# Kernel optimization log

Measured on AMD Instinct MI355X. Metric: run time of the kernel, lower is better.

The kernel has to match this reference:

```python
import jax, jax.numpy as jnp
import numpy as np

# model dims
B_, L_ = 2, 1024
D_MODEL = 768
N_LAYER = 6
VOCAB = 32000
MAX_POS = 2048
D_INNER = 2 * D_MODEL          # expand=2 (mamba default)
D_STATE = 16
D_CONV = 4
DT_RANK = (D_MODEL + 15) // 16 # ceil(d_model/16) = 48
EPS = 1e-5
D_EMB = D_MODEL // 2


def setup_inputs() -> dict:
    key = jax.random.key(0)
    ks = jax.random.split(key, 12)
    s = 0.02
    nl = N_LAYER
    A_init = jnp.tile(jnp.log(jnp.arange(1, D_STATE + 1, dtype=jnp.float32))[None, None, :], (nl, D_INNER, 1))
    return {
        "input_ids": jax.random.randint(ks[0], (B_, L_), 0, VOCAB),
        "position_ids": jax.random.randint(ks[1], (B_, L_), 0, MAX_POS),
        "emb_w": jax.random.normal(ks[2], (VOCAB, D_EMB), jnp.float32) * s,
        "pos_emb_w": jax.random.normal(ks[3], (MAX_POS, D_MODEL - D_EMB), jnp.float32) * s,
        "norm_w": jnp.ones((nl, D_MODEL), jnp.float32),
        "in_proj_w": jax.random.normal(ks[4], (nl, 2 * D_INNER, D_MODEL), jnp.float32) * s,
        "conv_w": jax.random.normal(ks[5], (nl, D_INNER, D_CONV), jnp.float32) * s,
        "conv_b": jnp.zeros((nl, D_INNER), jnp.float32),
        "x_proj_w": jax.random.normal(ks[6], (nl, DT_RANK + 2 * D_STATE, D_INNER), jnp.float32) * s,
        "dt_proj_w": jax.random.normal(ks[7], (nl, D_INNER, DT_RANK), jnp.float32) * s,
        "dt_proj_b": jax.random.normal(ks[8], (nl, D_INNER), jnp.float32) * s,
        "A_log": A_init,
        "D_vec": jnp.ones((nl, D_INNER), jnp.float32),
        "out_proj_w": jax.random.normal(ks[9], (nl, D_MODEL, D_INNER), jnp.float32) * s,
        "norm_f_w": jnp.ones((D_MODEL,), jnp.float32),
    }


def _rmsnorm(x, w, eps=EPS):
    x = x.astype(jnp.float32)
    return x * jax.lax.rsqrt(jnp.mean(x * x, axis=-1, keepdims=True) + eps) * w


def _causal_conv1d(x, w, b):
    # x: [B, L, D], w: [D, K] depthwise, b: [D]; causal left-pad K-1
    xT = jnp.transpose(x, (0, 2, 1))  # [B, D, L]
    out = jax.lax.conv_general_dilated(
        xT, w[:, None, :], window_strides=(1,), padding=[(w.shape[-1] - 1, 0)],
        dimension_numbers=("NCH", "OIH", "NCH"), feature_group_count=w.shape[0])
    return jnp.transpose(out, (0, 2, 1)) + b


def _selective_scan(x, dt, Bm, Cm, A, Dv):
    # x, dt: [B, L, Di]; Bm, Cm: [B, L, N]; A: [Di, N]; Dv: [Di]
    def step(h, inp):
        x_t, dt_t, B_t, C_t = inp  # [B,Di], [B,Di], [B,N], [B,N]
        dA = jnp.exp(dt_t[:, :, None] * A)                       # [B,Di,N], in (0,1]
        h = dA * h + dt_t[:, :, None] * B_t[:, None, :] * x_t[:, :, None]
        y = jnp.einsum("bdn,bn->bd", h, C_t)
        return h, y

    h0 = jnp.zeros((x.shape[0], A.shape[0], A.shape[1]), x.dtype)
    xs = (jnp.swapaxes(x, 0, 1), jnp.swapaxes(dt, 0, 1),
          jnp.swapaxes(Bm, 0, 1), jnp.swapaxes(Cm, 0, 1))
    _, ys = jax.lax.scan(step, h0, xs)
    return jnp.swapaxes(ys, 0, 1) + x * Dv


def _mamba_block(hidden, residual, p):
    # Block with fused_add_norm semantics: residual += hidden; h = RMSNorm(residual); h = Mamba(h)
    norm_w, in_w, cw, cb, xp_w, dtw, dtb, A_log, Dv, ow = p
    residual = hidden + residual
    hs = _rmsnorm(residual, norm_w)
    xz = jnp.einsum("bld,ed->ble", hs, in_w)      # [B,L,2*Di]
    x, z = jnp.split(xz, 2, axis=-1)
    x = jax.nn.silu(_causal_conv1d(x, cw, cb))
    x_dbl = jnp.einsum("bld,ed->ble", x, xp_w)     # [B,L,dt_rank+2N]
    dt = x_dbl[..., :DT_RANK]
    Bm = x_dbl[..., DT_RANK:DT_RANK + D_STATE]
    Cm = x_dbl[..., DT_RANK + D_STATE:]
    dt = jax.nn.softplus(jnp.einsum("blr,dr->bld", dt, dtw) + dtb)
    A = -jnp.exp(A_log)
    y = _selective_scan(x, dt, Bm, Cm, A, Dv)
    y = y * jax.nn.silu(z)
    return jnp.einsum("bld,ed->ble", y, ow), residual


def reference(input_ids, position_ids, emb_w, pos_emb_w, norm_w, in_proj_w, conv_w,
              conv_b, x_proj_w, dt_proj_w, dt_proj_b, A_log, D_vec, out_proj_w, norm_f_w):
    # token emb (d_model//2) || position emb (d_model - d_model//2)
    hidden = jnp.concatenate([emb_w[input_ids], pos_emb_w[position_ids]], axis=-1)
    residual = jnp.zeros_like(hidden)  # residual=None on first block == 0

    def layer_step(carry, p):
        h, r = carry
        h2, r2 = _mamba_block(h, r, p)
        return (h2, r2), None

    params = (norm_w, in_proj_w, conv_w, conv_b, x_proj_w, dt_proj_w, dt_proj_b,
              A_log, D_vec, out_proj_w)
    (hidden, residual), _ = jax.lax.scan(layer_step, (hidden, residual), params)
    hs = _rmsnorm(hidden + residual, norm_f_w)
    # LM head on first d_model//2 dims, weight tied to token embedding
    logits = jnp.einsum("bld,vd->blv", hs[..., :D_EMB], emb_w)
    return logits
```

## Files before the change

kernel.cpp:

```cpp
#include <hip/hip_runtime.h>
#include <math.h>

#define B_SZ 2
#define L_SZ 1024
#define BL (B_SZ * L_SZ)
#define D_MODEL 768
#define N_LAYER 6
#define VOCAB 32000
#define D_INNER 1536
#define D_STATE 16
#define D_CONV 4
#define DT_RANK 48
#define D_EMB 384
#define EPS 1e-5f

#define NCHUNK 64
#define CT 16
#define XD (DT_RANK + 2 * D_STATE)

typedef float vfloat4 __attribute__((ext_vector_type(4)));
typedef float f32x4  __attribute__((ext_vector_type(4)));
typedef short bf16x8 __attribute__((ext_vector_type(8)));

__device__ __forceinline__ float siluf(float x) {
    return x / (1.f + __expf(-x));
}

__global__ void embed_kernel(const int* __restrict__ ids, const int* __restrict__ pos,
                             const float* __restrict__ emb, const float* __restrict__ pemb,
                             float* __restrict__ hidden, float* __restrict__ residual) {
    int idx = blockIdx.x * blockDim.x + threadIdx.x;
    if (idx >= BL * D_MODEL) return;
    int c = idx % D_MODEL;
    int t = idx / D_MODEL;
    float v;
    if (c < D_EMB) v = emb[(size_t)ids[t] * D_EMB + c];
    else           v = pemb[(size_t)pos[t] * (D_MODEL - D_EMB) + (c - D_EMB)];
    hidden[idx] = v;
    residual[idx] = 0.f;
}

__global__ __launch_bounds__(256) void add_rmsnorm_kernel(
    const float* __restrict__ hidden, float* __restrict__ residual,
    const float* __restrict__ w, float* __restrict__ out) {
    int row = blockIdx.x;
    const float* h = hidden + (size_t)row * D_MODEL;
    float* r = residual + (size_t)row * D_MODEL;
    float* o = out + (size_t)row * D_MODEL;

    float v[3];
    float ss = 0.f;
#pragma unroll
    for (int i = 0; i < 3; i++) {
        int c = threadIdx.x + i * 256;
        float x = h[c] + r[c];
        v[i] = x;
        r[c] = x;
        ss += x * x;
    }
#pragma unroll
    for (int off = 32; off > 0; off >>= 1) ss += __shfl_down(ss, off, 64);
    __shared__ float parts[4];
    __shared__ float s_scale;
    int wid = threadIdx.x >> 6;
    int lane = threadIdx.x & 63;
    if (lane == 0) parts[wid] = ss;
    __syncthreads();
    if (threadIdx.x == 0) {
        float tot = parts[0] + parts[1] + parts[2] + parts[3];
        s_scale = rsqrtf(tot / (float)D_MODEL + EPS);
    }
    __syncthreads();
    float scale = s_scale;
#pragma unroll
    for (int i = 0; i < 3; i++) {
        int c = threadIdx.x + i * 256;
        o[c] = v[i] * scale * w[c];
    }
}

__global__ __launch_bounds__(256) void frag_convert_kernel(
    const float* __restrict__ src, int R, int ld, int Ksrc, int Kt,
    short* __restrict__ dh, short* __restrict__ dl) {
    int tile = blockIdx.x;
    int kt = tile % Kt, rt = tile / Kt;
    __shared__ float fs[128][65];
    int t = threadIdx.x;
    int rr = t >> 4;
    int c4 = (t & 15) * 4;
#pragma unroll
    for (int i = 0; i < 8; i++) {
        int rloc = rr + i * 16;
        int grow = rt * 128 + rloc;
        int gk = kt * 64 + c4;
        vfloat4 v = {0.f, 0.f, 0.f, 0.f};
        if (grow < R && gk < Ksrc)
            v = *(const vfloat4*)&src[(size_t)grow * ld + gk];
        fs[rloc][c4 + 0] = v[0];
        fs[rloc][c4 + 1] = v[1];
        fs[rloc][c4 + 2] = v[2];
        fs[rloc][c4 + 3] = v[3];
    }
    __syncthreads();
#pragma unroll
    for (int i = 0; i < 4; i++) {
        int o = t + i * 256;
        int sub = o >> 6, ln = o & 63;
        int r = (sub >> 1) * 16 + (ln & 15);
        int k = (sub & 1) * 32 + (ln >> 4) * 8;
        bf16x8 h, l;
#pragma unroll
        for (int j = 0; j < 8; j++) {
            float x = fs[r][k + j];
            unsigned u = __float_as_uint(x);
            h[j] = (short)(u >> 16);
            float res = x - __uint_as_float(u & 0xffff0000u);
            l[j] = (short)(__float_as_uint(res) >> 16);
        }
        size_t doff = (size_t)tile * 8192 + (size_t)o * 8;
        *(bf16x8*)&dh[doff] = h;
        *(bf16x8*)&dl[doff] = l;
    }
}

__device__ __forceinline__ void gload16(const short* g, short* l) {
    __builtin_amdgcn_global_load_lds(
        (const __attribute__((address_space(1))) void*)g,
        (__attribute__((address_space(3))) void*)l, 16, 0, 0);
}

__global__ __launch_bounds__(256, 2) void gemm_frag_kernel(
    const short* __restrict__ Af_h, const short* __restrict__ Af_l,
    const short* __restrict__ Bf_h, const short* __restrict__ Bf_l,
    const float* __restrict__ bias, float* __restrict__ C,
    int Mt, int Nt, int Kt, int N, int act, int ksplit) {

    __shared__ __align__(16) short smem[32768];

    const int tid  = threadIdx.x;
    const int lane = tid & 63;
    const int w    = tid >> 6;
    const int wm   = w >> 1, wn = w & 1;

    int nb  = Mt * Nt;
    int bid = blockIdx.x;
    int q = nb >> 3, r = nb & 7;
    int xcd = bid & 7, lin = bid >> 3;
    int wg = (xcd < r) ? (xcd * (q + 1) + lin) : (r * (q + 1) + (xcd - r) * q + lin);
    int mt = wg % Mt;
    int nt = wg / Mt;

    const int ktn = Kt / ksplit;
    const int kt0 = blockIdx.y * ktn;

    const short* ga_h = Af_h + ((size_t)mt * Kt + kt0) * 8192;
    const short* ga_l = Af_l + ((size_t)mt * Kt + kt0) * 8192;
    const short* gb_h = Bf_h + ((size_t)nt * Kt + kt0) * 8192;
    const short* gb_l = Bf_l + ((size_t)nt * Kt + kt0) * 8192;

    f32x4 acc[4][4];
#pragma unroll
    for (int i = 0; i < 4; i++)
#pragma unroll
        for (int j = 0; j < 4; j++)
            acc[i][j] = (f32x4){0.f, 0.f, 0.f, 0.f};

    for (int kk = 0; kk < ktn; kk++) {
        __syncthreads();
        {
            const size_t tb = (size_t)kk * 8192;
#pragma unroll
            for (int i = 0; i < 4; i++) {
                const int o = w * 2048 + i * 512;
                const int go = o + lane * 8;
                gload16(ga_h + tb + go, &smem[o]);
                gload16(ga_l + tb + go, &smem[8192  + o]);
                gload16(gb_h + tb + go, &smem[16384 + o]);
                gload16(gb_l + tb + go, &smem[24576 + o]);
            }
        }
        __syncthreads();

#pragma unroll
        for (int ksub = 0; ksub < 2; ksub++) {
            bf16x8 a_h[4], a_l[4], b_h[4], b_l[4];
#pragma unroll
            for (int mi = 0; mi < 4; mi++) {
                const int off = (((wm * 4 + mi) * 2 + ksub) * 64 + lane) * 8;
                a_h[mi] = *(const bf16x8*)&smem[off];
                a_l[mi] = *(const bf16x8*)&smem[8192 + off];
            }
#pragma unroll
            for (int ni = 0; ni < 4; ni++) {
                const int off = (((wn * 4 + ni) * 2 + ksub) * 64 + lane) * 8;
                b_h[ni] = *(const bf16x8*)&smem[16384 + off];
                b_l[ni] = *(const bf16x8*)&smem[24576 + off];
            }
#pragma unroll
            for (int mi = 0; mi < 4; mi++)
#pragma unroll
                for (int ni = 0; ni < 4; ni++) {
                    acc[mi][ni] = __builtin_amdgcn_mfma_f32_16x16x32_bf16(
                        a_h[mi], b_h[ni], acc[mi][ni], 0, 0, 0);
                    acc[mi][ni] = __builtin_amdgcn_mfma_f32_16x16x32_bf16(
                        a_h[mi], b_l[ni], acc[mi][ni], 0, 0, 0);
                    acc[mi][ni] = __builtin_amdgcn_mfma_f32_16x16x32_bf16(
                        a_l[mi], b_h[ni], acc[mi][ni], 0, 0, 0);
                }
        }
    }

    const int row0 = mt * 128 + wm * 64 + ((lane >> 4) << 2);
    const int col0 = nt * 128 + wn * 64 + (lane & 15);
    if (ksplit > 1) {
#pragma unroll
        for (int ni = 0; ni < 4; ni++) {
            const int col = col0 + ni * 16;
            if (col < N) {
#pragma unroll
                for (int mi = 0; mi < 4; mi++)
#pragma unroll
                    for (int rr = 0; rr < 4; rr++)
                        atomicAdd(&C[(size_t)(row0 + mi * 16 + rr) * N + col],
                                  acc[mi][ni][rr]);
            }
        }
    } else {
#pragma unroll
        for (int ni = 0; ni < 4; ni++) {
            const int col = col0 + ni * 16;
            if (col < N) {
                const float bv = bias ? bias[col] : 0.f;
#pragma unroll
                for (int mi = 0; mi < 4; mi++) {
#pragma unroll
                    for (int rr = 0; rr < 4; rr++) {
                        const int row = row0 + mi * 16 + rr;
                        float v = acc[mi][ni][rr] + bv;
                        if (act == 1) v = (v > 20.f) ? v : log1pf(__expf(v));
                        C[(size_t)row * N + col] = v;
                    }
                }
            }
        }
    }
}

__global__ void conv_silu_kernel(const float* __restrict__ xz,
                                 const float* __restrict__ cw,
                                 const float* __restrict__ cb,
                                 float* __restrict__ out) {
    int idx = blockIdx.x * blockDim.x + threadIdx.x;
    if (idx >= BL * D_INNER) return;
    int d = idx % D_INNER;
    int t = (idx / D_INNER) % L_SZ;
    int b = idx / (D_INNER * L_SZ);
    const float* xcol = xz + (size_t)b * L_SZ * (2 * D_INNER) + d;
    float s = cb[d];
#pragma unroll
    for (int j = 0; j < D_CONV; j++) {
        int li = t - (D_CONV - 1) + j;
        if (li >= 0) s += xcol[(size_t)li * (2 * D_INNER)] * cw[d * D_CONV + j];
    }
    out[idx] = siluf(s);
}

__global__ __launch_bounds__(256) void scan_passA_kernel(
    const float* __restrict__ xconv, const float* __restrict__ dt,
    const float* __restrict__ xdbl, const float* __restrict__ A_log,
    float* __restrict__ Pbuf, float* __restrict__ Sbuf) {
    int d = blockIdx.x * 256 + threadIdx.x;
    int c = blockIdx.y;
    int b = blockIdx.z;
    int t0 = c * CT;

    __shared__ float Bsh[CT][D_STATE];
    {
        int row = threadIdx.x >> 4, n = threadIdx.x & 15;
        Bsh[row][n] = xdbl[((size_t)(b * L_SZ + t0 + row)) * XD + DT_RANK + n];
    }
    __syncthreads();

    float A[D_STATE];
#pragma unroll
    for (int n = 0; n < D_STATE; n++) A[n] = -__expf(A_log[(size_t)d * D_STATE + n]);

    float P[D_STATE], S[D_STATE];
#pragma unroll
    for (int n = 0; n < D_STATE; n++) { P[n] = 1.f; S[n] = 0.f; }

    for (int t = 0; t < CT; t++) {
        size_t row = (size_t)b * L_SZ + t0 + t;
        float dtv = dt[row * D_INNER + d];
        float xv  = xconv[row * D_INNER + d];
#pragma unroll
        for (int n = 0; n < D_STATE; n++) {
            float dA = __expf(dtv * A[n]);
            P[n] *= dA;
            S[n] = dA * S[n] + dtv * Bsh[t][n] * xv;
        }
    }
    size_t base = (((size_t)b * NCHUNK + c) * D_INNER + d) * D_STATE;
#pragma unroll
    for (int n = 0; n < D_STATE; n++) { Pbuf[base + n] = P[n]; Sbuf[base + n] = S[n]; }
}

__global__ __launch_bounds__(256) void scan_passB_kernel(
    const float* __restrict__ Pbuf, const float* __restrict__ Sbuf,
    float* __restrict__ Hbuf) {
    int idx = blockIdx.x * 256 + threadIdx.x;
    int b = idx / (D_INNER * D_STATE);
    int dn = idx % (D_INNER * D_STATE);
    const int stride = D_INNER * D_STATE;
    size_t base = (size_t)b * NCHUNK * stride + dn;
    float H = 0.f;
#pragma unroll 8
    for (int c = 0; c < NCHUNK; c++) {
        size_t off = base + (size_t)c * stride;
        float p = Pbuf[off];
        float s = Sbuf[off];
        Hbuf[off] = H;
        H = p * H + s;
    }
}

__global__ __launch_bounds__(256) void scan_passC_kernel(
    const float* __restrict__ xconv, const float* __restrict__ dt,
    const float* __restrict__ xdbl, const float* __restrict__ A_log,
    const float* __restrict__ Dv, const float* __restrict__ xz,
    const float* __restrict__ Hin,
    float* __restrict__ y) {
    int d = blockIdx.x * 256 + threadIdx.x;
    int c = blockIdx.y;
    int b = blockIdx.z;
    int t0 = c * CT;

    __shared__ float BCsh[CT][2 * D_STATE];
#pragma unroll
    for (int i = 0; i < 2; i++) {
        int idx = threadIdx.x + i * 256;
        int row = idx >> 5, col = idx & 31;
        BCsh[row][col] = xdbl[((size_t)(b * L_SZ + t0 + row)) * XD + DT_RANK + col];
    }
    __syncthreads();

    float A[D_STATE];
#pragma unroll
    for (int n = 0; n < D_STATE; n++) A[n] = -__expf(A_log[(size_t)d * D_STATE + n]);
    float Dd = Dv[d];

    float h[D_STATE];
    size_t hbase = (((size_t)b * NCHUNK + c) * D_INNER + d) * D_STATE;
#pragma unroll
    for (int n = 0; n < D_STATE; n++) h[n] = Hin[hbase + n];

    for (int t = 0; t < CT; t++) {
        size_t row = (size_t)b * L_SZ + t0 + t;
        float dtv = dt[row * D_INNER + d];
        float xv  = xconv[row * D_INNER + d];
        float acc = 0.f;
#pragma unroll
        for (int n = 0; n < D_STATE; n++) {
            float dA = __expf(dtv * A[n]);
            h[n] = dA * h[n] + dtv * BCsh[t][n] * xv;
            acc += h[n] * BCsh[t][D_STATE + n];
        }
        acc += xv * Dd;
        float zv = xz[row * (2 * D_INNER) + D_INNER + d];
        y[row * D_INNER + d] = acc * siluf(zv);
    }
}

extern "C" void kernel_launch(void* const* d_in, const int* in_sizes, int n_in,
                              void* d_out, int out_size, void* d_ws, size_t ws_size,
                              hipStream_t stream) {
    const int*   input_ids    = (const int*)d_in[0];
    const int*   position_ids = (const int*)d_in[1];
    const float* emb_w        = (const float*)d_in[2];
    const float* pos_emb_w    = (const float*)d_in[3];
    const float* norm_w       = (const float*)d_in[4];
    const float* in_proj_w    = (const float*)d_in[5];
    const float* conv_w       = (const float*)d_in[6];
    const float* conv_b       = (const float*)d_in[7];
    const float* x_proj_w     = (const float*)d_in[8];
    const float* dt_proj_w    = (const float*)d_in[9];
    const float* dt_proj_b    = (const float*)d_in[10];
    const float* A_log        = (const float*)d_in[11];
    const float* D_vec        = (const float*)d_in[12];
    const float* out_proj_w   = (const float*)d_in[13];
    const float* norm_f_w     = (const float*)d_in[14];
    float* logits = (float*)d_out;

    float* ws = (float*)d_ws;
    float* hidden   = ws; ws += (size_t)BL * D_MODEL;
    float* residual = ws; ws += (size_t)BL * D_MODEL;
    float* hs       = ws; ws += (size_t)BL * D_MODEL;
    float* xz       = ws; ws += (size_t)BL * 2 * D_INNER;
    float* xconv    = ws; ws += (size_t)BL * D_INNER;
    float* xdbl     = ws; ws += (size_t)BL * XD;
    float* dtbuf    = ws; ws += (size_t)BL * D_INNER;
    float* ybuf     = ws; ws += (size_t)BL * D_INNER;
    float* Pbuf     = ws; ws += (size_t)B_SZ * NCHUNK * D_INNER * D_STATE;
    float* Sbuf     = ws; ws += (size_t)B_SZ * NCHUNK * D_INNER * D_STATE;
    float* Hbuf     = ws; ws += (size_t)B_SZ * NCHUNK * D_INNER * D_STATE;

    short* sp = (short*)ws;
    auto salloc = [&](size_t n) { short* p = sp; sp += n; return p; };
    const int KT_DM  = D_MODEL / 64;
    const int KT_DI  = D_INNER / 64;
    const int KT_EMB = D_EMB / 64;
    short* embf_h = salloc((size_t)(VOCAB/128) * KT_EMB * 8192);
    short* embf_l = salloc((size_t)(VOCAB/128) * KT_EMB * 8192);
    short* iwf_h  = salloc((size_t)(2*D_INNER/128) * KT_DM * 8192);
    short* iwf_l  = salloc((size_t)(2*D_INNER/128) * KT_DM * 8192);
    short* xpf_h  = salloc((size_t)1 * KT_DI * 8192);
    short* xpf_l  = salloc((size_t)1 * KT_DI * 8192);
    short* dtwf_h = salloc((size_t)(D_INNER/128) * 1 * 8192);
    short* dtwf_l = salloc((size_t)(D_INNER/128) * 1 * 8192);
    short* owf_h  = salloc((size_t)(D_MODEL/128) * KT_DI * 8192);
    short* owf_l  = salloc((size_t)(D_MODEL/128) * KT_DI * 8192);
    short* hsf_h  = salloc((size_t)(BL/128) * KT_DM * 8192);
    short* hsf_l  = salloc((size_t)(BL/128) * KT_DM * 8192);
    short* xcf_h  = salloc((size_t)(BL/128) * KT_DI * 8192);
    short* xcf_l  = salloc((size_t)(BL/128) * KT_DI * 8192);
    short* x48f_h = salloc((size_t)(BL/128) * 1 * 8192);
    short* x48f_l = salloc((size_t)(BL/128) * 1 * 8192);
    short* yf_h   = salloc((size_t)(BL/128) * KT_DI * 8192);
    short* yf_l   = salloc((size_t)(BL/128) * KT_DI * 8192);

    auto conv_frag = [&](const float* src, int R, int ld, int Ksrc, int Rt, int Kt,
                         short* dh, short* dl) {
        frag_convert_kernel<<<Rt * Kt, 256, 0, stream>>>(src, R, ld, Ksrc, Kt, dh, dl);
    };
    auto gemm = [&](const short* Ah, const short* Al, const short* Bh, const short* Bl,
                    const float* bias, float* C, int Mt, int Nt, int Kt, int N,
                    int act, int ksplit) {
        dim3 grid(Mt * Nt, ksplit);
        gemm_frag_kernel<<<grid, 256, 0, stream>>>(Ah, Al, Bh, Bl, bias, C,
                                                   Mt, Nt, Kt, N, act, ksplit);
    };

    embed_kernel<<<(BL * D_MODEL + 255) / 256, 256, 0, stream>>>(
        input_ids, position_ids, emb_w, pos_emb_w, hidden, residual);

    conv_frag(emb_w, VOCAB, D_EMB, D_EMB, VOCAB / 128, KT_EMB, embf_h, embf_l);

    for (int l = 0; l < N_LAYER; l++) {
        const float* nw  = norm_w     + (size_t)l * D_MODEL;
        const float* iw  = in_proj_w  + (size_t)l * 2 * D_INNER * D_MODEL;
        const float* cw  = conv_w     + (size_t)l * D_INNER * D_CONV;
        const float* cb  = conv_b     + (size_t)l * D_INNER;
        const float* xpw = x_proj_w   + (size_t)l * XD * D_INNER;
        const float* dtw = dt_proj_w  + (size_t)l * D_INNER * DT_RANK;
        const float* dtb = dt_proj_b  + (size_t)l * D_INNER;
        const float* al  = A_log      + (size_t)l * D_INNER * D_STATE;
        const float* dv  = D_vec      + (size_t)l * D_INNER;
        const float* ow  = out_proj_w + (size_t)l * D_MODEL * D_INNER;

        add_rmsnorm_kernel<<<BL, 256, 0, stream>>>(hidden, residual, nw, hs);
        conv_frag(hs, BL, D_MODEL, D_MODEL, BL / 128, KT_DM, hsf_h, hsf_l);
        conv_frag(iw, 2 * D_INNER, D_MODEL, D_MODEL, 2 * D_INNER / 128, KT_DM,
                  iwf_h, iwf_l);

        gemm(hsf_h, hsf_l, iwf_h, iwf_l, nullptr, xz,
             BL / 128, 2 * D_INNER / 128, KT_DM, 2 * D_INNER, 0, 1);

        conv_silu_kernel<<<(BL * D_INNER + 255) / 256, 256, 0, stream>>>(xz, cw, cb, xconv);
        conv_frag(xconv, BL, D_INNER, D_INNER, BL / 128, KT_DI, xcf_h, xcf_l);
        conv_frag(xpw, XD, D_INNER, D_INNER, 1, KT_DI, xpf_h, xpf_l);

        hipMemsetAsync(xdbl, 0, (size_t)BL * XD * sizeof(float), stream);
        gemm(xcf_h, xcf_l, xpf_h, xpf_l, nullptr, xdbl,
             BL / 128, 1, KT_DI, XD, 0, 8);

        conv_frag(xdbl, BL, XD, DT_RANK, BL / 128, 1, x48f_h, x48f_l);
        conv_frag(dtw, D_INNER, DT_RANK, DT_RANK, D_INNER / 128, 1, dtwf_h, dtwf_l);
        gemm(x48f_h, x48f_l, dtwf_h, dtwf_l, dtb, dtbuf,
             BL / 128, D_INNER / 128, 1, D_INNER, 1, 1);

        {
            dim3 gA(D_INNER / 256, NCHUNK, B_SZ);
            scan_passA_kernel<<<gA, 256, 0, stream>>>(xconv, dtbuf, xdbl, al, Pbuf, Sbuf);
            scan_passB_kernel<<<(B_SZ * D_INNER * D_STATE) / 256, 256, 0, stream>>>(
                Pbuf, Sbuf, Hbuf);
            scan_passC_kernel<<<gA, 256, 0, stream>>>(xconv, dtbuf, xdbl, al, dv, xz,
                                                      Hbuf, ybuf);
        }

        conv_frag(ybuf, BL, D_INNER, D_INNER, BL / 128, KT_DI, yf_h, yf_l);
        conv_frag(ow, D_MODEL, D_INNER, D_INNER, D_MODEL / 128, KT_DI, owf_h, owf_l);
        hipMemsetAsync(hidden, 0, (size_t)BL * D_MODEL * sizeof(float), stream);
        gemm(yf_h, yf_l, owf_h, owf_l, nullptr, hidden,
             BL / 128, D_MODEL / 128, KT_DI, D_MODEL, 0, 2);
    }

    add_rmsnorm_kernel<<<BL, 256, 0, stream>>>(hidden, residual, norm_f_w, hs);
    conv_frag(hs, BL, D_MODEL, D_EMB, BL / 128, KT_EMB, hsf_h, hsf_l);

    gemm(hsf_h, hsf_l, embf_h, embf_l, nullptr, logits,
         BL / 128, VOCAB / 128, KT_EMB, VOCAB, 0, 1);
}
```

Baseline: 1.904 ms.

## Halve GEMM K-tile to raise occupancy and batch per-layer weight conversions

The GEMM K-step drops from 64 to 32, which halves the shared-memory tile and lets the launch bound allow 4 blocks per CU instead of 2. The fragment layout is re-indexed to match. The x_proj and dt_proj weight conversions are hoisted out of the layer loop into one batched launch across all layers. The xdbl memset is folded into the conv_silu kernel, and out_proj uses split-K 4. In exchange, each K step now needs twice as many barriers and global-to-LDS rounds, and split-K 4 adds more atomics.

```diff
diff --git a/kernel.cpp b/kernel.cpp
--- a/kernel.cpp
+++ b/kernel.cpp
@@ -80,10 +80,17 @@
 }
 
 __global__ __launch_bounds__(256) void frag_convert_kernel(
-    const float* __restrict__ src, int R, int ld, int Ksrc, int Kt,
+    const float* __restrict__ src, int R, int ld, int Ksrc, int Kt64,
+    size_t src_lstride, size_t dst_lstride,
     short* __restrict__ dh, short* __restrict__ dl) {
     int tile = blockIdx.x;
-    int kt = tile % Kt, rt = tile / Kt;
+    int lyr = blockIdx.y;
+    const float* s = src + (size_t)lyr * src_lstride;
+    short* dhp = dh + (size_t)lyr * dst_lstride;
+    short* dlp = dl + (size_t)lyr * dst_lstride;
+    int kt = tile % Kt64, rt = tile / Kt64;
+    const int K32 = Kt64 * 2;
+
     __shared__ float fs[128][65];
     int t = threadIdx.x;
     int rr = t >> 4;
@@ -95,7 +102,7 @@
         int gk = kt * 64 + c4;
         vfloat4 v = {0.f, 0.f, 0.f, 0.f};
         if (grow < R && gk < Ksrc)
-            v = *(const vfloat4*)&src[(size_t)grow * ld + gk];
+            v = *(const vfloat4*)&s[(size_t)grow * ld + gk];
         fs[rloc][c4 + 0] = v[0];
         fs[rloc][c4 + 1] = v[1];
         fs[rloc][c4 + 2] = v[2];
@@ -106,8 +113,9 @@
     for (int i = 0; i < 4; i++) {
         int o = t + i * 256;
         int sub = o >> 6, ln = o & 63;
-        int r = (sub >> 1) * 16 + (ln & 15);
-        int k = (sub & 1) * 32 + (ln >> 4) * 8;
+        int msub = sub >> 1, ksub = sub & 1;
+        int r = msub * 16 + (ln & 15);
+        int k = ksub * 32 + (ln >> 4) * 8;
         bf16x8 h, l;
 #pragma unroll
         for (int j = 0; j < 8; j++) {
@@ -117,9 +125,10 @@
             float res = x - __uint_as_float(u & 0xffff0000u);
             l[j] = (short)(__float_as_uint(res) >> 16);
         }
-        size_t doff = (size_t)tile * 8192 + (size_t)o * 8;
-        *(bf16x8*)&dh[doff] = h;
-        *(bf16x8*)&dl[doff] = l;
+        size_t doff = ((size_t)rt * K32 + kt * 2 + ksub) * 4096
+                    + (size_t)(msub * 64 + ln) * 8;
+        *(bf16x8*)&dhp[doff] = h;
+        *(bf16x8*)&dlp[doff] = l;
     }
 }
 
@@ -129,13 +138,13 @@
         (__attribute__((address_space(3))) void*)l, 16, 0, 0);
 }
 
-__global__ __launch_bounds__(256, 2) void gemm_frag_kernel(
+__global__ __launch_bounds__(256, 4) void gemm_frag_kernel(
     const short* __restrict__ Af_h, const short* __restrict__ Af_l,
     const short* __restrict__ Bf_h, const short* __restrict__ Bf_l,
     const float* __restrict__ bias, float* __restrict__ C,
-    int Mt, int Nt, int Kt, int N, int act, int ksplit) {
-
-    __shared__ __align__(16) short smem[32768];
+    int Mt, int Nt, int K32, int N, int act, int ksplit) {
+
+    __shared__ __align__(16) short smem[16384];
 
     const int tid  = threadIdx.x;
     const int lane = tid & 63;
@@ -150,13 +159,13 @@
     int mt = wg % Mt;
     int nt = wg / Mt;
 
-    const int ktn = Kt / ksplit;
+    const int ktn = K32 / ksplit;
     const int kt0 = blockIdx.y * ktn;
 
-    const short* ga_h = Af_h + ((size_t)mt * Kt + kt0) * 8192;
-    const short* ga_l = Af_l + ((size_t)mt * Kt + kt0) * 8192;
-    const short* gb_h = Bf_h + ((size_t)nt * Kt + kt0) * 8192;
-    const short* gb_l = Bf_l + ((size_t)nt * Kt + kt0) * 8192;
+    const short* ga_h = Af_h + ((size_t)mt * K32 + kt0) * 4096;
+    const short* ga_l = Af_l + ((size_t)mt * K32 + kt0) * 4096;
+    const short* gb_h = Bf_h + ((size_t)nt * K32 + kt0) * 4096;
+    const short* gb_l = Bf_l + ((size_t)nt * K32 + kt0) * 4096;
 
     f32x4 acc[4][4];
 #pragma unroll
@@ -168,46 +177,43 @@
     for (int kk = 0; kk < ktn; kk++) {
         __syncthreads();
         {
-            const size_t tb = (size_t)kk * 8192;
-#pragma unroll
-            for (int i = 0; i < 4; i++) {
-                const int o = w * 2048 + i * 512;
+            const size_t tb = (size_t)kk * 4096;
+#pragma unroll
+            for (int i = 0; i < 2; i++) {
+                const int o = w * 1024 + i * 512;
                 const int go = o + lane * 8;
                 gload16(ga_h + tb + go, &smem[o]);
-                gload16(ga_l + tb + go, &smem[8192  + o]);
-                gload16(gb_h + tb + go, &smem[16384 + o]);
-                gload16(gb_l + tb + go, &smem[24576 + o]);
+                gload16(ga_l + tb + go, &smem[4096  + o]);
+                gload16(gb_h + tb + go, &smem[8192  + o]);
+                gload16(gb_l + tb + go, &smem[12288 + o]);
             }
         }
         __syncthreads();
 
-#pragma unroll
-        for (int ksub = 0; ksub < 2; ksub++) {
-            bf16x8 a_h[4], a_l[4], b_h[4], b_l[4];
-#pragma unroll
-            for (int mi = 0; mi < 4; mi++) {
-                const int off = (((wm * 4 + mi) * 2 + ksub) * 64 + lane) * 8;
-                a_h[mi] = *(const bf16x8*)&smem[off];
-                a_l[mi] = *(const bf16x8*)&smem[8192 + off];
+        bf16x8 a_h[4], a_l[4], b_h[4], b_l[4];
+#pragma unroll
+        for (int mi = 0; mi < 4; mi++) {
+            const int off = ((wm * 4 + mi) * 64 + lane) * 8;
+            a_h[mi] = *(const bf16x8*)&smem[off];
+            a_l[mi] = *(const bf16x8*)&smem[4096 + off];
+        }
+#pragma unroll
+        for (int ni = 0; ni < 4; ni++) {
+            const int off = ((wn * 4 + ni) * 64 + lane) * 8;
+            b_h[ni] = *(const bf16x8*)&smem[8192 + off];
+            b_l[ni] = *(const bf16x8*)&smem[12288 + off];
+        }
+#pragma unroll
+        for (int mi = 0; mi < 4; mi++)
+#pragma unroll
+            for (int ni = 0; ni < 4; ni++) {
+                acc[mi][ni] = __builtin_amdgcn_mfma_f32_16x16x32_bf16(
+                    a_h[mi], b_h[ni], acc[mi][ni], 0, 0, 0);
+                acc[mi][ni] = __builtin_amdgcn_mfma_f32_16x16x32_bf16(
+                    a_h[mi], b_l[ni], acc[mi][ni], 0, 0, 0);
+                acc[mi][ni] = __builtin_amdgcn_mfma_f32_16x16x32_bf16(
+                    a_l[mi], b_h[ni], acc[mi][ni], 0, 0, 0);
             }
-#pragma unroll
-            for (int ni = 0; ni < 4; ni++) {
-                const int off = (((wn * 4 + ni) * 2 + ksub) * 64 + lane) * 8;
-                b_h[ni] = *(const bf16x8*)&smem[16384 + off];
-                b_l[ni] = *(const bf16x8*)&smem[24576 + off];
-            }
-#pragma unroll
-            for (int mi = 0; mi < 4; mi++)
-#pragma unroll
-                for (int ni = 0; ni < 4; ni++) {
-                    acc[mi][ni] = __builtin_amdgcn_mfma_f32_16x16x32_bf16(
-                        a_h[mi], b_h[ni], acc[mi][ni], 0, 0, 0);
-                    acc[mi][ni] = __builtin_amdgcn_mfma_f32_16x16x32_bf16(
-                        a_h[mi], b_l[ni], acc[mi][ni], 0, 0, 0);
-                    acc[mi][ni] = __builtin_amdgcn_mfma_f32_16x16x32_bf16(
-                        a_l[mi], b_h[ni], acc[mi][ni], 0, 0, 0);
-                }
-        }
     }
 
     const int row0 = mt * 128 + wm * 64 + ((lane >> 4) << 2);
@@ -249,9 +255,11 @@
 __global__ void conv_silu_kernel(const float* __restrict__ xz,
                                  const float* __restrict__ cw,
                                  const float* __restrict__ cb,
-                                 float* __restrict__ out) {
+                                 float* __restrict__ out,
+                                 float* __restrict__ xdbl_zero) {
     int idx = blockIdx.x * blockDim.x + threadIdx.x;
     if (idx >= BL * D_INNER) return;
+    if (idx < BL * XD) xdbl_zero[idx] = 0.f;
     int d = idx % D_INNER;
     int t = (idx / D_INNER) % L_SZ;
     int b = idx / (D_INNER * L_SZ);
@@ -406,77 +414,82 @@
 
     short* sp = (short*)ws;
     auto salloc = [&](size_t n) { short* p = sp; sp += n; return p; };
-    const int KT_DM  = D_MODEL / 64;
-    const int KT_DI  = D_INNER / 64;
-    const int KT_EMB = D_EMB / 64;
-    short* embf_h = salloc((size_t)(VOCAB/128) * KT_EMB * 8192);
-    short* embf_l = salloc((size_t)(VOCAB/128) * KT_EMB * 8192);
-    short* iwf_h  = salloc((size_t)(2*D_INNER/128) * KT_DM * 8192);
-    short* iwf_l  = salloc((size_t)(2*D_INNER/128) * KT_DM * 8192);
-    short* xpf_h  = salloc((size_t)1 * KT_DI * 8192);
-    short* xpf_l  = salloc((size_t)1 * KT_DI * 8192);
-    short* dtwf_h = salloc((size_t)(D_INNER/128) * 1 * 8192);
-    short* dtwf_l = salloc((size_t)(D_INNER/128) * 1 * 8192);
-    short* owf_h  = salloc((size_t)(D_MODEL/128) * KT_DI * 8192);
-    short* owf_l  = salloc((size_t)(D_MODEL/128) * KT_DI * 8192);
-    short* hsf_h  = salloc((size_t)(BL/128) * KT_DM * 8192);
-    short* hsf_l  = salloc((size_t)(BL/128) * KT_DM * 8192);
-    short* xcf_h  = salloc((size_t)(BL/128) * KT_DI * 8192);
-    short* xcf_l  = salloc((size_t)(BL/128) * KT_DI * 8192);
-    short* x48f_h = salloc((size_t)(BL/128) * 1 * 8192);
-    short* x48f_l = salloc((size_t)(BL/128) * 1 * 8192);
-    short* yf_h   = salloc((size_t)(BL/128) * KT_DI * 8192);
-    short* yf_l   = salloc((size_t)(BL/128) * KT_DI * 8192);
-
-    auto conv_frag = [&](const float* src, int R, int ld, int Ksrc, int Rt, int Kt,
-                         short* dh, short* dl) {
-        frag_convert_kernel<<<Rt * Kt, 256, 0, stream>>>(src, R, ld, Ksrc, Kt, dh, dl);
+    const int K32_DM  = D_MODEL / 32;
+    const int K32_DI  = D_INNER / 32;
+    const int K32_EMB = D_EMB / 32;
+    const size_t XPF_L  = (size_t)1 * K32_DI * 4096;
+    const size_t DTWF_L = (size_t)(D_INNER / 128) * 2 * 4096;
+    short* embf_h = salloc((size_t)(VOCAB/128) * K32_EMB * 4096);
+    short* embf_l = salloc((size_t)(VOCAB/128) * K32_EMB * 4096);
+    short* iwf_h  = salloc((size_t)(2*D_INNER/128) * K32_DM * 4096);
+    short* iwf_l  = salloc((size_t)(2*D_INNER/128) * K32_DM * 4096);
+    short* xpf_h  = salloc(XPF_L * N_LAYER);
+    short* xpf_l  = salloc(XPF_L * N_LAYER);
+    short* dtwf_h = salloc(DTWF_L * N_LAYER);
+    short* dtwf_l = salloc(DTWF_L * N_LAYER);
+    short* owf_h  = salloc((size_t)(D_MODEL/128) * K32_DI * 4096);
+    short* owf_l  = salloc((size_t)(D_MODEL/128) * K32_DI * 4096);
+    short* hsf_h  = salloc((size_t)(BL/128) * K32_DM * 4096);
+    short* hsf_l  = salloc((size_t)(BL/128) * K32_DM * 4096);
+    short* xcf_h  = salloc((size_t)(BL/128) * K32_DI * 4096);
+    short* xcf_l  = salloc((size_t)(BL/128) * K32_DI * 4096);
+    short* x48f_h = salloc((size_t)(BL/128) * 2 * 4096);
+    short* x48f_l = salloc((size_t)(BL/128) * 2 * 4096);
+    short* yf_h   = salloc((size_t)(BL/128) * K32_DI * 4096);
+    short* yf_l   = salloc((size_t)(BL/128) * K32_DI * 4096);
+
+    auto conv_frag = [&](const float* src, int R, int ld, int Ksrc, int Rt, int Kt64,
+                         short* dh, short* dl, int layers = 1,
+                         size_t sstr = 0, size_t dstr = 0) {
+        dim3 grid(Rt * Kt64, layers);
+        frag_convert_kernel<<<grid, 256, 0, stream>>>(src, R, ld, Ksrc, Kt64,
+                                                      sstr, dstr, dh, dl);
     };
     auto gemm = [&](const short* Ah, const short* Al, const short* Bh, const short* Bl,
-                    const float* bias, float* C, int Mt, int Nt, int Kt, int N,
+                    const float* bias, float* C, int Mt, int Nt, int K32, int N,
                     int act, int ksplit) {
         dim3 grid(Mt * Nt, ksplit);
         gemm_frag_kernel<<<grid, 256, 0, stream>>>(Ah, Al, Bh, Bl, bias, C,
-                                                   Mt, Nt, Kt, N, act, ksplit);
+                                                   Mt, Nt, K32, N, act, ksplit);
     };
 
     embed_kernel<<<(BL * D_MODEL + 255) / 256, 256, 0, stream>>>(
         input_ids, position_ids, emb_w, pos_emb_w, hidden, residual);
 
-    conv_frag(emb_w, VOCAB, D_EMB, D_EMB, VOCAB / 128, KT_EMB, embf_h, embf_l);
+    conv_frag(emb_w, VOCAB, D_EMB, D_EMB, VOCAB / 128, D_EMB / 64, embf_h, embf_l);
+    conv_frag(x_proj_w, XD, D_INNER, D_INNER, 1, D_INNER / 64, xpf_h, xpf_l,
+              N_LAYER, (size_t)XD * D_INNER, XPF_L);
+    conv_frag(dt_proj_w, D_INNER, DT_RANK, DT_RANK, D_INNER / 128, 1, dtwf_h, dtwf_l,
+              N_LAYER, (size_t)D_INNER * DT_RANK, DTWF_L);
 
     for (int l = 0; l < N_LAYER; l++) {
         const float* nw  = norm_w     + (size_t)l * D_MODEL;
         const float* iw  = in_proj_w  + (size_t)l * 2 * D_INNER * D_MODEL;
         const float* cw  = conv_w     + (size_t)l * D_INNER * D_CONV;
         const float* cb  = conv_b     + (size_t)l * D_INNER;
-        const float* xpw = x_proj_w   + (size_t)l * XD * D_INNER;
-        const float* dtw = dt_proj_w  + (size_t)l * D_INNER * DT_RANK;
         const float* dtb = dt_proj_b  + (size_t)l * D_INNER;
         const float* al  = A_log      + (size_t)l * D_INNER * D_STATE;
         const float* dv  = D_vec      + (size_t)l * D_INNER;
         const float* ow  = out_proj_w + (size_t)l * D_MODEL * D_INNER;
 
         add_rmsnorm_kernel<<<BL, 256, 0, stream>>>(hidden, residual, nw, hs);
-        conv_frag(hs, BL, D_MODEL, D_MODEL, BL / 128, KT_DM, hsf_h, hsf_l);
-        conv_frag(iw, 2 * D_INNER, D_MODEL, D_MODEL, 2 * D_INNER / 128, KT_DM,
+        conv_frag(hs, BL, D_MODEL, D_MODEL, BL / 128, D_MODEL / 64, hsf_h, hsf_l);
+        conv_frag(iw, 2 * D_INNER, D_MODEL, D_MODEL, 2 * D_INNER / 128, D_MODEL / 64,
                   iwf_h, iwf_l);
 
         gemm(hsf_h, hsf_l, iwf_h, iwf_l, nullptr, xz,
-             BL / 128, 2 * D_INNER / 128, KT_DM, 2 * D_INNER, 0, 1);
-
-        conv_silu_kernel<<<(BL * D_INNER + 255) / 256, 256, 0, stream>>>(xz, cw, cb, xconv);
-        conv_frag(xconv, BL, D_INNER, D_INNER, BL / 128, KT_DI, xcf_h, xcf_l);
-        conv_frag(xpw, XD, D_INNER, D_INNER, 1, KT_DI, xpf_h, xpf_l);
-
-        hipMemsetAsync(xdbl, 0, (size_t)BL * XD * sizeof(float), stream);
-        gemm(xcf_h, xcf_l, xpf_h, xpf_l, nullptr, xdbl,
-             BL / 128, 1, KT_DI, XD, 0, 8);
+             BL / 128, 2 * D_INNER / 128, K32_DM, 2 * D_INNER, 0, 1);
+
+        conv_silu_kernel<<<(BL * D_INNER + 255) / 256, 256, 0, stream>>>(
+            xz, cw, cb, xconv, xdbl);
+        conv_frag(xconv, BL, D_INNER, D_INNER, BL / 128, D_INNER / 64, xcf_h, xcf_l);
+
+        gemm(xcf_h, xcf_l, xpf_h + l * XPF_L, xpf_l + l * XPF_L, nullptr, xdbl,
+             BL / 128, 1, K32_DI, XD, 0, 8);
 
         conv_frag(xdbl, BL, XD, DT_RANK, BL / 128, 1, x48f_h, x48f_l);
-        conv_frag(dtw, D_INNER, DT_RANK, DT_RANK, D_INNER / 128, 1, dtwf_h, dtwf_l);
-        gemm(x48f_h, x48f_l, dtwf_h, dtwf_l, dtb, dtbuf,
-             BL / 128, D_INNER / 128, 1, D_INNER, 1, 1);
+        gemm(x48f_h, x48f_l, dtwf_h + l * DTWF_L, dtwf_l + l * DTWF_L, dtb, dtbuf,
+             BL / 128, D_INNER / 128, 2, D_INNER, 1, 1);
 
         {
             dim3 gA(D_INNER / 256, NCHUNK, B_SZ);
@@ -487,16 +500,17 @@
                                                       Hbuf, ybuf);
         }
 
-        conv_frag(ybuf, BL, D_INNER, D_INNER, BL / 128, KT_DI, yf_h, yf_l);
-        conv_frag(ow, D_MODEL, D_INNER, D_INNER, D_MODEL / 128, KT_DI, owf_h, owf_l);
+        conv_frag(ybuf, BL, D_INNER, D_INNER, BL / 128, D_INNER / 64, yf_h, yf_l);
+        conv_frag(ow, D_MODEL, D_INNER, D_INNER, D_MODEL / 128, D_INNER / 64,
+                  owf_h, owf_l);
         hipMemsetAsync(hidden, 0, (size_t)BL * D_MODEL * sizeof(float), stream);
         gemm(yf_h, yf_l, owf_h, owf_l, nullptr, hidden,
-             BL / 128, D_MODEL / 128, KT_DI, D_MODEL, 0, 2);
+             BL / 128, D_MODEL / 128, K32_DI, D_MODEL, 0, 4);
     }
 
     add_rmsnorm_kernel<<<BL, 256, 0, stream>>>(hidden, residual, norm_f_w, hs);
-    conv_frag(hs, BL, D_MODEL, D_EMB, BL / 128, KT_EMB, hsf_h, hsf_l);
+    conv_frag(hs, BL, D_MODEL, D_EMB, BL / 128, D_EMB / 64, hsf_h, hsf_l);
 
     gemm(hsf_h, hsf_l, embf_h, embf_l, nullptr, logits,
-         BL / 128, VOCAB / 128, KT_EMB, VOCAB, 0, 1);
-}
+         BL / 128, VOCAB / 128, K32_EMB, VOCAB, 0, 1);
+}
```

Measured after the change: 1.846 ms. -3.1%, faster.
